# Performance work log

Hardware: AMD Instinct MI355X
Metric: run time of the kernel (lower is better)

The kernel has to match this reference:

```python
import jax, jax.numpy as jnp
import numpy as np

NEG_SLOPE = 0.2  # GATConv default negative_slope

def setup_inputs() -> dict:
    key = jax.random.key(0)
    k1, k2, k3, k4 = jax.random.split(key, 4)
    N, Cin, Cout = 2048, 128, 64
    return {
        "data": jax.random.normal(k1, (N, Cin), jnp.float32),
        "W": jax.random.normal(k2, (Cin, Cout), jnp.float32) / np.sqrt(Cin).astype(np.float32),
        "att_src": jax.random.normal(k3, (Cout,), jnp.float32) * 0.1,
        "att_dst": jax.random.normal(k4, (Cout,), jnp.float32) * 0.1,
        "bias": jnp.zeros((Cout,), jnp.float32),
    }

def reference(data, W, att_src, att_dst, bias):
    N = data.shape[0]
    # torch.combinations(arange(N)).t(): edges (i, j) with i < j, src=i, dst=j
    rows, cols = jnp.triu_indices(N, k=1)
    loop = jnp.arange(N)  # GATConv add_self_loops=True
    src = jnp.concatenate([rows, loop])
    dst = jnp.concatenate([cols, loop])

    h = data @ W                       # [N, Cout]
    a_s = h @ att_src                  # [N]
    a_d = h @ att_dst                  # [N]

    # per-edge attention logits, leaky_relu, segment softmax over dst
    e = jax.nn.leaky_relu(a_s[src] + a_d[dst], NEG_SLOPE)          # [E]
    m = jax.ops.segment_max(e, dst, num_segments=N)                # [N]
    ex = jnp.exp(e - m[dst])                                       # [E]
    denom = jax.ops.segment_sum(ex, dst, num_segments=N)           # [N]
    alpha = ex / denom[dst]                                        # [E]

    # scatter-add weighted source features
    out = jax.ops.segment_sum(alpha[:, None] * h[src], dst, num_segments=N) + bias
    return jax.nn.relu(out)
```

## Files before the change

### kernel.cpp

```cpp
#include <hip/hip_runtime.h>
#include <hip/hip_bf16.h>
#include <math.h>

#define N 2048
#define CIN 128
#define COUT 64
#define NEG 0.2f
#define JB 16
#define NJB (N / JB)

typedef __attribute__((ext_vector_type(8))) short short8;
typedef __attribute__((ext_vector_type(4))) float f32x4;

__device__ __forceinline__ ushort bf16u(float x) {
  __hip_bfloat16 b = __float2bfloat16(x);
  return *reinterpret_cast<ushort*>(&b);
}
__device__ __forceinline__ uint pack2(float lo, float hi) {
  return (uint)bf16u(lo) | ((uint)bf16u(hi) << 16);
}

__global__ __launch_bounds__(1024) void gat_gemm_mfma(
    const float* __restrict__ data, const float* __restrict__ W,
    const float* __restrict__ att_src, const float* __restrict__ att_dst,
    ushort* __restrict__ hfrag, float* __restrict__ a_s,
    float* __restrict__ a_d) {
  const int tid = (int)threadIdx.x;
  const int i0 = (int)blockIdx.x * 64;

  __shared__ ushort abuf[16 * 64 * 8];
  __shared__ ushort wbuf[16 * 64 * 8];
  __shared__ float asp[4 * 64];
  __shared__ float adp[4 * 64];

  {
    const int mi = tid >> 8, kc = (tid >> 6) & 3, L = tid & 63;
    const int row = i0 + mi * 16 + (L & 15);
    const int col = kc * 32 + (L >> 4) * 8;
    const float4 f0 = *(const float4*)&data[row * CIN + col];
    const float4 f1 = *(const float4*)&data[row * CIN + col + 4];
    uint4 pa;
    pa.x = pack2(f0.x, f0.y);
    pa.y = pack2(f0.z, f0.w);
    pa.z = pack2(f1.x, f1.y);
    pa.w = pack2(f1.z, f1.w);
    *(uint4*)&abuf[tid * 8] = pa;
  }
  {
    const int kc = tid >> 8, cf = (tid >> 6) & 3, L = tid & 63;
    const int krow = kc * 32 + (L >> 4) * 8;
    const int c = cf * 16 + (L & 15);
    ushort uw[8];
#pragma unroll
    for (int e = 0; e < 8; ++e) uw[e] = bf16u(W[(krow + e) * COUT + c]);
    uint4 pw;
    pw.x = (uint)uw[0] | ((uint)uw[1] << 16);
    pw.y = (uint)uw[2] | ((uint)uw[3] << 16);
    pw.z = (uint)uw[4] | ((uint)uw[5] << 16);
    pw.w = (uint)uw[6] | ((uint)uw[7] << 16);
    *(uint4*)&wbuf[tid * 8] = pw;
  }
  __syncthreads();

  const int w = tid >> 6, lane = tid & 63;
  const int mi = w >> 2, ci = w & 3;
  f32x4 acc = {0.f, 0.f, 0.f, 0.f};
#pragma unroll
  for (int kc = 0; kc < 4; ++kc) {
    const short8 a = *(const short8*)&abuf[((mi * 4 + kc) * 64 + lane) * 8];
    const short8 b = *(const short8*)&wbuf[((kc * 4 + ci) * 64 + lane) * 8];
    acc = __builtin_amdgcn_mfma_f32_16x16x32_bf16(a, b, acc, 0, 0, 0);
  }

  const int q = lane >> 4;
  const int colg = ci * 16 + (lane & 15);
  const float sc = att_src[colg];
  const float dc = att_dst[colg];
  float ps[4], pd[4];
#pragma unroll
  for (int r = 0; r < 4; ++r) { ps[r] = acc[r] * sc; pd[r] = acc[r] * dc; }
#pragma unroll
  for (int off = 1; off < 16; off <<= 1) {
#pragma unroll
    for (int r = 0; r < 4; ++r) {
      ps[r] += __shfl_xor(ps[r], off);
      pd[r] += __shfl_xor(pd[r], off);
    }
  }
  if ((lane & 15) == 0) {
#pragma unroll
    for (int r = 0; r < 4; ++r) {
      asp[ci * 64 + mi * 16 + q * 4 + r] = ps[r];
      adp[ci * 64 + mi * 16 + q * 4 + r] = pd[r];
    }
  }
  {
    const int ib = i0 + mi * 16 + q * 4;
    const int f = (ib >> 5) * 4 + ci;
    const int lp = ((ib >> 3) & 3) * 16 + (lane & 15);
    uint2 hv;
    hv.x = pack2(acc[0], acc[1]);
    hv.y = pack2(acc[2], acc[3]);
    *(uint2*)&hfrag[((size_t)(f * 64 + lp) << 3) + (ib & 7)] = hv;
  }
  __syncthreads();
  if (tid < 64) {
    a_s[i0 + tid] = asp[tid] + asp[64 + tid] + asp[128 + tid] + asp[192 + tid];
    a_d[i0 + tid] = adp[tid] + adp[64 + tid] + adp[128 + tid] + adp[192 + tid];
  }
}

__global__ __launch_bounds__(1024) void gat_attn_flash(
    const ushort* __restrict__ hfrag, const float* __restrict__ a_s,
    const float* __restrict__ a_d, const float* __restrict__ bias,
    float* __restrict__ out) {
  const int bj = NJB - 1 - (int)blockIdx.x;
  const int tid = (int)threadIdx.x;
  const int wid = tid >> 6;
  const int lane = tid & 63;
  const int j0 = bj * JB;
  const int jme = j0 + (lane & 15);
  const int kgrp = lane >> 4;
  const float ad_me = a_d[jme];
  const int nks = (bj + 2) >> 1;

  f32x4 acc0 = {0.f, 0.f, 0.f, 0.f};
  f32x4 acc1 = acc0, acc2 = acc0, acc3 = acc0;
  float dsum = 0.f;
  const uint4* hf = (const uint4*)hfrag;

  for (int ks = wid; ks < nks; ks += 16) {
    const int ibase = ks * 32 + kgrp * 8;
    const float4 asa = *(const float4*)&a_s[ibase];
    const float4 asb = *(const float4*)&a_s[ibase + 4];
    const float av[8] = {asa.x, asa.y, asa.z, asa.w,
                         asb.x, asb.y, asb.z, asb.w};
    short8 af;
#pragma unroll
    for (int e = 0; e < 8; ++e) {
      float x = av[e] + ad_me;
      x = fmaxf(x, NEG * x);
      float wgt = __expf(x);
      if (ibase + e > jme) wgt = 0.f;
      dsum += wgt;
      af[e] = (short)bf16u(wgt);
    }
    const int fbase = (ks * 4) * 64 + lane;
    const uint4 b0 = hf[fbase];
    const uint4 b1 = hf[fbase + 64];
    const uint4 b2 = hf[fbase + 128];
    const uint4 b3 = hf[fbase + 192];
    acc0 = __builtin_amdgcn_mfma_f32_16x16x32_bf16(af, *(const short8*)&b0,
                                                   acc0, 0, 0, 0);
    acc1 = __builtin_amdgcn_mfma_f32_16x16x32_bf16(af, *(const short8*)&b1,
                                                   acc1, 0, 0, 0);
    acc2 = __builtin_amdgcn_mfma_f32_16x16x32_bf16(af, *(const short8*)&b2,
                                                   acc2, 0, 0, 0);
    acc3 = __builtin_amdgcn_mfma_f32_16x16x32_bf16(af, *(const short8*)&b3,
                                                   acc3, 0, 0, 0);
  }

  dsum += __shfl_xor(dsum, 16);
  dsum += __shfl_xor(dsum, 32);

  __shared__ float rbuf[16][16][64];
  __shared__ float dbuf[16][16];
#pragma unroll
  for (int r = 0; r < 4; ++r) {
    rbuf[0 + r][wid][lane]  = acc0[r];
    rbuf[4 + r][wid][lane]  = acc1[r];
    rbuf[8 + r][wid][lane]  = acc2[r];
    rbuf[12 + r][wid][lane] = acc3[r];
  }
  if (lane < 16) dbuf[wid][lane] = dsum;
  __syncthreads();

  {
    const int j = tid >> 6, c = tid & 63;
    const int qq = j >> 2, rr = j & 3, t16 = c >> 4, n = c & 15;
    float num = 0.f, den = 0.f;
#pragma unroll
    for (int ww = 0; ww < 16; ++ww) {
      num += rbuf[t16 * 4 + rr][ww][qq * 16 + n];
      den += dbuf[ww][j];
    }
    const float v = num / den + bias[c];
    out[(size_t)(j0 + j) * COUT + c] = v > 0.f ? v : 0.f;
  }
}

extern "C" void kernel_launch(void* const* d_in, const int* in_sizes, int n_in,
                              void* d_out, int out_size, void* d_ws, size_t ws_size,
                              hipStream_t stream) {
  const float* data    = (const float*)d_in[0];
  const float* W       = (const float*)d_in[1];
  const float* att_src = (const float*)d_in[2];
  const float* att_dst = (const float*)d_in[3];
  const float* bias    = (const float*)d_in[4];
  float* out = (float*)d_out;

  ushort* hfrag = (ushort*)d_ws;
  float* a_s  = (float*)d_ws + 65536;
  float* a_d  = a_s + N;

  gat_gemm_mfma<<<N / 64, 1024, 0, stream>>>(data, W, att_src, att_dst,
                                             hfrag, a_s, a_d);
  gat_attn_flash<<<NJB, 1024, 0, stream>>>(hfrag, a_s, a_d, bias, out);
}
```

Before: 15.42 us.

## Split GEMM into 16-row blocks and load MFMA operands directly to registers

The projection GEMM now launches 128 blocks of 256 threads, each computing 16 rows, instead of 32 blocks of 1024 threads computing 64 rows. Each wave loads its A and W fragments straight from global memory into registers, so the shared-memory staging and the barrier before the MFMAs are gone. This spreads the small GEMM over more compute units. The cost is that every block reloads and re-converts the W tile, which adds redundant global reads.

```diff
diff --git a/kernel.cpp b/kernel.cpp
--- a/kernel.cpp
+++ b/kernel.cpp
@@ -20,93 +20,88 @@
   return (uint)bf16u(lo) | ((uint)bf16u(hi) << 16);
 }
 
-__global__ __launch_bounds__(1024) void gat_gemm_mfma(
+__global__ __launch_bounds__(256) void gat_gemm_mfma(
     const float* __restrict__ data, const float* __restrict__ W,
     const float* __restrict__ att_src, const float* __restrict__ att_dst,
     ushort* __restrict__ hfrag, float* __restrict__ a_s,
     float* __restrict__ a_d) {
   const int tid = (int)threadIdx.x;
-  const int i0 = (int)blockIdx.x * 64;
-
-  __shared__ ushort abuf[16 * 64 * 8];
-  __shared__ ushort wbuf[16 * 64 * 8];
-  __shared__ float asp[4 * 64];
-  __shared__ float adp[4 * 64];
-
-  {
-    const int mi = tid >> 8, kc = (tid >> 6) & 3, L = tid & 63;
-    const int row = i0 + mi * 16 + (L & 15);
-    const int col = kc * 32 + (L >> 4) * 8;
-    const float4 f0 = *(const float4*)&data[row * CIN + col];
-    const float4 f1 = *(const float4*)&data[row * CIN + col + 4];
+  const int ci = tid >> 6;
+  const int lane = tid & 63;
+  const int i0 = (int)blockIdx.x * 16;
+  const int q = lane >> 4;
+  const int n15 = lane & 15;
+  const int mrow = i0 + n15;
+
+  short8 af[4];
+#pragma unroll
+  for (int kc = 0; kc < 4; ++kc) {
+    const int col = kc * 32 + q * 8;
+    const float4 f0 = *(const float4*)&data[mrow * CIN + col];
+    const float4 f1 = *(const float4*)&data[mrow * CIN + col + 4];
     uint4 pa;
     pa.x = pack2(f0.x, f0.y);
     pa.y = pack2(f0.z, f0.w);
     pa.z = pack2(f1.x, f1.y);
     pa.w = pack2(f1.z, f1.w);
-    *(uint4*)&abuf[tid * 8] = pa;
-  }
-  {
-    const int kc = tid >> 8, cf = (tid >> 6) & 3, L = tid & 63;
-    const int krow = kc * 32 + (L >> 4) * 8;
-    const int c = cf * 16 + (L & 15);
+    af[kc] = *(short8*)&pa;
+  }
+
+  const int cg = ci * 16 + n15;
+  f32x4 acc = {0.f, 0.f, 0.f, 0.f};
+#pragma unroll
+  for (int kc = 0; kc < 4; ++kc) {
+    const int kr = kc * 32 + q * 8;
     ushort uw[8];
 #pragma unroll
-    for (int e = 0; e < 8; ++e) uw[e] = bf16u(W[(krow + e) * COUT + c]);
+    for (int e = 0; e < 8; ++e) uw[e] = bf16u(W[(kr + e) * COUT + cg]);
     uint4 pw;
     pw.x = (uint)uw[0] | ((uint)uw[1] << 16);
     pw.y = (uint)uw[2] | ((uint)uw[3] << 16);
     pw.z = (uint)uw[4] | ((uint)uw[5] << 16);
     pw.w = (uint)uw[6] | ((uint)uw[7] << 16);
-    *(uint4*)&wbuf[tid * 8] = pw;
-  }
-  __syncthreads();
-
-  const int w = tid >> 6, lane = tid & 63;
-  const int mi = w >> 2, ci = w & 3;
-  f32x4 acc = {0.f, 0.f, 0.f, 0.f};
-#pragma unroll
-  for (int kc = 0; kc < 4; ++kc) {
-    const short8 a = *(const short8*)&abuf[((mi * 4 + kc) * 64 + lane) * 8];
-    const short8 b = *(const short8*)&wbuf[((kc * 4 + ci) * 64 + lane) * 8];
-    acc = __builtin_amdgcn_mfma_f32_16x16x32_bf16(a, b, acc, 0, 0, 0);
-  }
-
-  const int q = lane >> 4;
-  const int colg = ci * 16 + (lane & 15);
-  const float sc = att_src[colg];
-  const float dc = att_dst[colg];
-  float ps[4], pd[4];
-#pragma unroll
-  for (int r = 0; r < 4; ++r) { ps[r] = acc[r] * sc; pd[r] = acc[r] * dc; }
-#pragma unroll
-  for (int off = 1; off < 16; off <<= 1) {
-#pragma unroll
-    for (int r = 0; r < 4; ++r) {
-      ps[r] += __shfl_xor(ps[r], off);
-      pd[r] += __shfl_xor(pd[r], off);
-    }
-  }
-  if ((lane & 15) == 0) {
-#pragma unroll
-    for (int r = 0; r < 4; ++r) {
-      asp[ci * 64 + mi * 16 + q * 4 + r] = ps[r];
-      adp[ci * 64 + mi * 16 + q * 4 + r] = pd[r];
-    }
-  }
+    acc = __builtin_amdgcn_mfma_f32_16x16x32_bf16(af[kc], *(short8*)&pw,
+                                                  acc, 0, 0, 0);
+  }
+
   {
-    const int ib = i0 + mi * 16 + q * 4;
+    const int ib = i0 + q * 4;
     const int f = (ib >> 5) * 4 + ci;
-    const int lp = ((ib >> 3) & 3) * 16 + (lane & 15);
+    const int lp = ((ib >> 3) & 3) * 16 + n15;
     uint2 hv;
     hv.x = pack2(acc[0], acc[1]);
     hv.y = pack2(acc[2], acc[3]);
     *(uint2*)&hfrag[((size_t)(f * 64 + lp) << 3) + (ib & 7)] = hv;
   }
+
+  __shared__ float asp[4][16];
+  __shared__ float adp[4][16];
+  {
+    const float sc = att_src[cg];
+    const float dc = att_dst[cg];
+    float ps[4], pd[4];
+#pragma unroll
+    for (int r = 0; r < 4; ++r) { ps[r] = acc[r] * sc; pd[r] = acc[r] * dc; }
+#pragma unroll
+    for (int off = 1; off < 16; off <<= 1) {
+#pragma unroll
+      for (int r = 0; r < 4; ++r) {
+        ps[r] += __shfl_xor(ps[r], off);
+        pd[r] += __shfl_xor(pd[r], off);
+      }
+    }
+    if (n15 == 0) {
+#pragma unroll
+      for (int r = 0; r < 4; ++r) {
+        asp[ci][q * 4 + r] = ps[r];
+        adp[ci][q * 4 + r] = pd[r];
+      }
+    }
+  }
   __syncthreads();
-  if (tid < 64) {
-    a_s[i0 + tid] = asp[tid] + asp[64 + tid] + asp[128 + tid] + asp[192 + tid];
-    a_d[i0 + tid] = adp[tid] + adp[64 + tid] + adp[128 + tid] + adp[192 + tid];
+  if (tid < 16) {
+    a_s[i0 + tid] = asp[0][tid] + asp[1][tid] + asp[2][tid] + asp[3][tid];
+    a_d[i0 + tid] = adp[0][tid] + adp[1][tid] + adp[2][tid] + adp[3][tid];
   }
 }
 
@@ -203,7 +198,7 @@
   float* a_s  = (float*)d_ws + 65536;
   float* a_d  = a_s + N;
 
-  gat_gemm_mfma<<<N / 64, 1024, 0, stream>>>(data, W, att_src, att_dst,
-                                             hfrag, a_s, a_d);
+  gat_gemm_mfma<<<N / 16, 256, 0, stream>>>(data, W, att_src, att_dst,
+                                            hfrag, a_s, a_d);
   gat_attn_flash<<<NJB, 1024, 0, stream>>>(hfrag, a_s, a_d, bias, out);
 }
```

After: 15.11 us. -2.0%, faster.
